# Kernel optimization log

Hardware: AMD Instinct MI355X
Metric: run time of the kernel (lower is better)

## Reference

```python
import jax, jax.numpy as jnp
import numpy as np

WS = 8      # window size
SS = 4      # shift size
NH = 4      # num heads
EPS = 1e-5
MLP_RATIO = 4


def _win_part(x, ws):
    # x: [B,D,H,W,C] -> [B*nD*nH*nW, ws^3, C]
    B, D, H, W, C = x.shape
    x = x.reshape(B, D // ws, ws, H // ws, ws, W // ws, ws, C)
    x = x.transpose(0, 1, 3, 5, 2, 4, 6, 7)
    return x.reshape(-1, ws * ws * ws, C)


def _win_rev(w, ws, B, D, H, W):
    C = w.shape[-1]
    x = w.reshape(B, D // ws, H // ws, W // ws, ws, ws, ws, C)
    x = x.transpose(0, 1, 4, 2, 5, 3, 6, 7)
    return x.reshape(B, D, H, W, C)


def _ln(x, g, b):
    m = jnp.mean(x, axis=-1, keepdims=True)
    v = jnp.mean((x - m) ** 2, axis=-1, keepdims=True)
    return (x - m) / jnp.sqrt(v + EPS) * g + b


def _rel_index(ws):
    coords = np.stack(np.meshgrid(np.arange(ws), np.arange(ws), np.arange(ws), indexing='ij'))  # [3,ws,ws,ws]
    cf = coords.reshape(3, -1)                      # [3, ws^3]
    rel = (cf[:, :, None] - cf[:, None, :]).transpose(1, 2, 0) + (ws - 1)  # [N,N,3]
    return rel[..., 0] * (2 * ws - 1) ** 2 + rel[..., 1] * (2 * ws - 1) + rel[..., 2]


def _attn_mask(D, H, W, ws, ss):
    img = np.zeros((1, D, H, W, 1), dtype=np.float32)
    cnt = 0
    sl = (slice(0, -ws), slice(-ws, -ss), slice(-ss, None))
    for d in sl:
        for h in sl:
            for w in sl:
                img[:, d, h, w, :] = cnt
                cnt += 1
    mw = np.asarray(_win_part(jnp.asarray(img), ws))[..., 0]  # [nW, ws^3]
    diff = mw[:, None, :] - mw[:, :, None]
    return np.where(diff != 0, -100.0, 0.0).astype(np.float32)


def setup_inputs() -> dict:
    key = jax.random.key(0)
    ks = jax.random.split(key, 12)
    B, D, H, W, C = 1, 16, 64, 64, 128
    mh = MLP_RATIO * C
    s = 0.02
    return {
        'x': jax.random.normal(ks[0], (B, D, H, W, C), jnp.float32),
        'attn_mask': jnp.asarray(_attn_mask(D, H, W, WS, SS)),
        'rel_index': jnp.asarray(_rel_index(WS), jnp.int32),
        'rel_bias': jax.random.normal(ks[1], ((2 * WS - 1) ** 3, NH), jnp.float32) * s,
        'qkv_w': jax.random.normal(ks[2], (3 * C, C), jnp.float32) * s,
        'qkv_b': jnp.zeros((3 * C,), jnp.float32),
        'proj_w': jax.random.normal(ks[3], (C, C), jnp.float32) * s,
        'proj_b': jnp.zeros((C,), jnp.float32),
        'norm1_g': jnp.ones((C,), jnp.float32),
        'norm1_b': jnp.zeros((C,), jnp.float32),
        'norm2_g': jnp.ones((C,), jnp.float32),
        'norm2_b': jnp.zeros((C,), jnp.float32),
        'mlp_w1': jax.random.normal(ks[4], (mh, C), jnp.float32) * s,
        'mlp_b1': jnp.zeros((mh,), jnp.float32),
        'mlp_w2': jax.random.normal(ks[5], (C, mh), jnp.float32) * s,
        'mlp_b2': jnp.zeros((C,), jnp.float32),
    }


def reference(x, attn_mask, rel_index, rel_bias, qkv_w, qkv_b, proj_w, proj_b,
              norm1_g, norm1_b, norm2_g, norm2_b, mlp_w1, mlp_b1, mlp_w2, mlp_b2):
    B, D, H, W, C = x.shape
    ws, ss, nh = WS, SS, NH
    hd = C // nh
    scale = hd ** -0.5
    N = ws ** 3
    shortcut = x
    h = _ln(x, norm1_g, norm1_b)
    h = jnp.roll(h, (-ss, -ss, -ss), axis=(1, 2, 3))
    xw = _win_part(h, ws)                 # [B_, N, C]
    B_ = xw.shape[0]
    nW = attn_mask.shape[0]
    qkv = xw @ qkv_w.T + qkv_b            # [B_, N, 3C]
    qkv = qkv.reshape(B_, N, 3, nh, hd).transpose(2, 0, 3, 1, 4)  # [3,B_,h,N,hd]
    q, k, v = qkv[0] * scale, qkv[1], qkv[2]
    attn = jnp.einsum('bhnd,bhmd->bhnm', q, k)
    rpe = rel_bias[rel_index.reshape(-1)].reshape(N, N, nh).transpose(2, 0, 1)  # [h,N,N]
    attn = attn + rpe[None]
    attn = attn.reshape(B_ // nW, nW, nh, N, N) + attn_mask[None, :, None]
    attn = jax.nn.softmax(attn.reshape(B_, nh, N, N), axis=-1)
    out = jnp.einsum('bhnm,bhmd->bhnd', attn, v).transpose(0, 2, 1, 3).reshape(B_, N, C)
    out = out @ proj_w.T + proj_b
    out = _win_rev(out, ws, B, D, H, W)
    out = jnp.roll(out, (ss, ss, ss), axis=(1, 2, 3))
    x = shortcut + out
    h2 = _ln(x, norm2_g, norm2_b)
    h2 = jax.nn.gelu(h2 @ mlp_w1.T + mlp_b1, approximate=False)
    return x + h2 @ mlp_w2.T + mlp_b2
```

## Files before the change

kernel.cpp:

```cpp
#include <hip/hip_runtime.h>
#include <math.h>

typedef __bf16 bf16;
typedef __bf16 bf16x4 __attribute__((ext_vector_type(4)));
typedef __bf16 bf16x8 __attribute__((ext_vector_type(8)));
typedef float f32x4 __attribute__((ext_vector_type(4)));
typedef unsigned short u16;
typedef u16 u16x2 __attribute__((ext_vector_type(2)));

#define LOG2E 1.4426950408889634f

__device__ __forceinline__ float b2f(u16 b) {
  return (float)__builtin_bit_cast(bf16, b);
}

__global__ void sniff_k(const unsigned* __restrict__ xw_, int* __restrict__ flag) {
  int lane = threadIdx.x;
  int c = 0;
#pragma unroll
  for (int j = 0; j < 4; j++) {
    unsigned e = (xw_[lane * 4 + j] >> 7) & 0xFFu;
    c += (e >= 100u && e <= 140u) ? 1 : 0;
  }
#pragma unroll
  for (int d = 1; d < 64; d <<= 1) c += __shfl_xor(c, d);
  if (lane == 0) *flag = (c >= 150) ? 1 : 0;
}

__global__ __launch_bounds__(256) void canon_big_k(const void* __restrict__ src,
                                                   bf16* __restrict__ dst,
                                                   const int* __restrict__ flag) {
  int i = (blockIdx.x * 256 + threadIdx.x) * 8;
  if (*flag) {
    *(bf16x8*)&dst[i] = *(const bf16x8*)((const bf16*)src + i);
  } else {
    const float* s = (const float*)src + i;
    bf16x8 v;
#pragma unroll
    for (int j = 0; j < 8; j++) v[j] = (bf16)s[j];
    *(bf16x8*)&dst[i] = v;
  }
}

struct CanonArgs {
  const void* src[13];
  bf16* dst[13];
  int n[13];
};

__global__ __launch_bounds__(256) void canon_small_k(CanonArgs a,
                                                     const int* __restrict__ flag) {
  int ti = blockIdx.y;
  int i = blockIdx.x * 256 + threadIdx.x;
  if (i >= a.n[ti]) return;
  if (*flag)
    a.dst[ti][i] = ((const bf16*)a.src[ti])[i];
  else
    a.dst[ti][i] = (bf16)((const float*)a.src[ti])[i];
}

__global__ __launch_bounds__(256) void rpem_k(const int* __restrict__ ridx,
                                              const bf16* __restrict__ rbias,
                                              bf16* __restrict__ rpem) {
  int t = blockIdx.x * 256 + threadIdx.x;
  int m0 = (t & 127) * 4, q = (t >> 7) & 511, h = (t >> 16) & 3, ty = t >> 18;
  int qd = q >> 6, qh = (q >> 3) & 7, qw = q & 7;
  int4 ri = *(const int4*)&ridx[q * 512 + m0];
  const int rv[4] = {ri.x, ri.y, ri.z, ri.w};
  bf16x4 o;
#pragma unroll
  for (int j = 0; j < 4; j++) {
    int m = m0 + j;
    int md = m >> 6, mh = (m >> 3) & 7, mw = m & 7;
    bool diff = ((ty & 4) && ((qd < 4) != (md < 4))) ||
                ((ty & 2) && ((qh < 4) != (mh < 4))) ||
                ((ty & 1) && ((qw < 4) != (mw < 4)));
    float v = (float)rbias[rv[j] * 4 + h] * LOG2E;
    o[j] = (bf16)(v + (diff ? -144.2695041f : 0.f));
  }
  *(bf16x4*)&rpem[(size_t)t * 4] = o;
}

template <int ROLL>
__global__ __launch_bounds__(256) void ln_k(const bf16* __restrict__ x,
                                            const bf16* __restrict__ g,
                                            const bf16* __restrict__ bsh,
                                            bf16* __restrict__ out) {
  int wave = threadIdx.x >> 6, lane = threadIdx.x & 63;
  int tok = blockIdx.x * 4 + wave;
  size_t src;
  if (ROLL) {
    int win = tok >> 9, pos = tok & 511;
    int rd = (win >> 6) * 8 + (pos >> 6);
    int rh = ((win >> 3) & 7) * 8 + ((pos >> 3) & 7);
    int rw = (win & 7) * 8 + (pos & 7);
    int od = (rd + 4) & 15, oh = (rh + 4) & 63, ow = (rw + 4) & 63;
    src = (size_t)((od * 64 + oh) * 64 + ow) * 128;
  } else {
    src = (size_t)tok * 128;
  }
  int ch = lane * 2;
  u16x2 xv = *(const u16x2*)(x + src + ch);
  float f0 = b2f(xv[0]), f1 = b2f(xv[1]);
  float s = f0 + f1, sq = f0 * f0 + f1 * f1;
#pragma unroll
  for (int d = 1; d < 64; d <<= 1) {
    s += __shfl_xor(s, d);
    sq += __shfl_xor(sq, d);
  }
  float mean = s * (1.f / 128.f);
  float var = sq * (1.f / 128.f) - mean * mean;
  float rstd = rsqrtf(fmaxf(var, 0.f) + 1e-5f);
  u16x2 gv = *(const u16x2*)(g + ch), bv = *(const u16x2*)(bsh + ch);
  u16x2 ov;
  ov[0] = __builtin_bit_cast(u16, (bf16)((f0 - mean) * rstd * b2f(gv[0]) + b2f(bv[0])));
  ov[1] = __builtin_bit_cast(u16, (bf16)((f1 - mean) * rstd * b2f(gv[1]) + b2f(bv[1])));
  *(u16x2*)(out + (size_t)tok * 128 + ch) = ov;
}

template <int EPI, int BM, int N_, int K_>
__global__ __launch_bounds__(256) void gemm_k(const bf16* __restrict__ A,
                                              const bf16* __restrict__ B,
                                              const bf16* __restrict__ bias,
                                              void* __restrict__ outv,
                                              const bf16* __restrict__ resid,
                                              const int* __restrict__ flag) {
  __shared__ __align__(16) u16 As[BM * 72];
  __shared__ __align__(16) u16 Bs[128 * 72];
  const int t = threadIdx.x;
  const int wave = t >> 6, lane = t & 63, l15 = lane & 15, quad = lane >> 4;
  const int m0 = blockIdx.x * BM, n0 = blockIdx.y * 128;
  constexpr int MI = BM / 32;
  constexpr int PA = BM / 32;
  int fl = 0;
  if constexpr (EPI == 3) fl = *flag;
  f32x4 acc[MI][4] = {};
  const int wr = (wave >> 1) * (BM / 2), wc = (wave & 1) * 64;
  const int srow = t >> 3, scol = (t & 7) * 8;
  constexpr int NC = K_ / 64;
  bf16x8 avA[PA], avB[PA];
#pragma unroll
  for (int p = 0; p < PA; p++) {
    int row = p * 32 + srow;
    avA[p] = *(const bf16x8*)(A + (size_t)(m0 + row) * K_ + scol);
  }
#pragma unroll
  for (int c = 0; c < NC; c++) {
    const bf16x8* av = (c & 1) ? avB : avA;
    bf16x8* avN = (c & 1) ? avA : avB;
    if (c + 1 < NC) {
#pragma unroll
      for (int p = 0; p < PA; p++) {
        int row = p * 32 + srow;
        avN[p] = *(const bf16x8*)(A + (size_t)(m0 + row) * K_ + (c + 1) * 64 + scol);
      }
    }
    bf16x8 bv[4];
#pragma unroll
    for (int p = 0; p < 4; p++) {
      int row = p * 32 + srow;
      bv[p] = *(const bf16x8*)(B + (size_t)(n0 + row) * K_ + c * 64 + scol);
    }
    __syncthreads();
#pragma unroll
    for (int p = 0; p < PA; p++)
      *(bf16x8*)&As[(p * 32 + srow) * 72 + scol] = av[p];
#pragma unroll
    for (int p = 0; p < 4; p++)
      *(bf16x8*)&Bs[(p * 32 + srow) * 72 + scol] = bv[p];
    __syncthreads();
#pragma unroll
    for (int ks = 0; ks < 2; ks++) {
      bf16x8 a[MI], b[4];
#pragma unroll
      for (int i = 0; i < MI; i++)
        a[i] = *(const bf16x8*)&As[(wr + i * 16 + l15) * 72 + ks * 32 + quad * 8];
#pragma unroll
      for (int j = 0; j < 4; j++)
        b[j] = *(const bf16x8*)&Bs[(wc + j * 16 + l15) * 72 + ks * 32 + quad * 8];
#pragma unroll
      for (int i = 0; i < MI; i++)
#pragma unroll
        for (int j = 0; j < 4; j++)
          acc[i][j] =
              __builtin_amdgcn_mfma_f32_16x16x32_bf16(a[i], b[j], acc[i][j], 0, 0, 0);
    }
  }
  const float qscale = 0.17677669529663687f * LOG2E;
#pragma unroll
  for (int i = 0; i < MI; i++) {
#pragma unroll
    for (int r = 0; r < 4; r++) {
      int tok = m0 + wr + i * 16 + quad * 4 + r;
      size_t obase = 0;
      if constexpr (EPI == 1) {
        int win = tok >> 9, pos = tok & 511;
        int rd = (win >> 6) * 8 + (pos >> 6);
        int rh = ((win >> 3) & 7) * 8 + ((pos >> 3) & 7);
        int rw = (win & 7) * 8 + (pos & 7);
        int od = (rd + 4) & 15, oh = (rh + 4) & 63, ow = (rw + 4) & 63;
        obase = (size_t)((od * 64 + oh) * 64 + ow) * 128;
      } else if constexpr (EPI != 0) {
        obase = (size_t)tok * N_;
      }
#pragma unroll
      for (int j = 0; j < 4; j++) {
        int gn = n0 + wc + j * 16 + l15;
        float v = acc[i][j][r] + (float)bias[gn];
        if constexpr (EPI == 0) {
          int tensor = gn >> 7, c = gn & 127, head = c >> 5, d = c & 31;
          if (tensor == 0) v *= qscale;
          int win = tok >> 9, pos = tok & 511;
          size_t off = ((((size_t)tensor * 4 + head) * 128 + win) * 512 + pos) * 32 + d;
          ((bf16*)outv)[off] = (bf16)v;
        } else if constexpr (EPI == 1) {
          v += (float)resid[obase + gn];
          ((bf16*)outv)[obase + gn] = (bf16)v;
        } else if constexpr (EPI == 2) {
          float v2 = v * v;
          float u2 = v * (2.30220806f + 0.10294323f * v2);
          float e2 = exp2f(u2);
          float rcp = __builtin_amdgcn_rcpf(e2 + 1.f);
          v = v - v * rcp;
          ((bf16*)outv)[obase + gn] = (bf16)v;
        } else {
          v += (float)resid[obase + gn];
          if (fl)
            ((bf16*)outv)[obase + gn] = (bf16)v;
          else
            ((float*)outv)[obase + gn] = v;
        }
      }
    }
  }
}

__global__ __launch_bounds__(512, 4) void attn_k(const bf16* __restrict__ qkv,
                                                 const bf16* __restrict__ rpem,
                                                 bf16* __restrict__ att) {
  __shared__ __align__(16) bf16 sVt[32 * 512];
  __shared__ __align__(16) bf16 sP[8][32 * 64];
  const int t = threadIdx.x;
  const int p = blockIdx.x;
  const int win = ((p >> 6) << 3) | (p & 7);
  const int mid = (p >> 3) & 7;
  const int head = mid >> 1, qh = mid & 1;
  const int wave = t >> 6, lane = t & 63, l15 = lane & 15, quad = lane >> 4;

  const int wd = win >> 6, wh = (win >> 3) & 7, ww = win & 7;
  const int type = ((wd == 1) << 2) | ((wh == 7) << 1) | (ww == 7);

  const size_t hw32 = (size_t)512 * 32;
  const bf16* qp = qkv + ((size_t)(0 * 4 + head) * 128 + win) * hw32;
  const bf16* kp = qkv + ((size_t)(1 * 4 + head) * 128 + win) * hw32;
  const bf16* vp = qkv + ((size_t)(2 * 4 + head) * 128 + win) * hw32;
  const bf16* rpeh = rpem + (size_t)(type * 4 + head) * 512 * 512;
  const int qbase = qh * 256 + wave * 32;

  {
    int kpi = t >> 3, dblk = (t & 7) * 4;
    char* sb = (char*)sVt;
#pragma unroll
    for (int kb = 0; kb < 4; kb++) {
      const bf16* v0 = vp + (size_t)(kb * 128 + 2 * kpi) * 32 + dblk;
      bf16x4 a = *(const bf16x4*)v0;
      bf16x4 b = *(const bf16x4*)(v0 + 32);
      int keyw = kb * 64 + kpi;
#pragma unroll
      for (int dd = 0; dd < 4; dd++) {
        int row = dblk + dd;
        unsigned wv = (unsigned)__builtin_bit_cast(u16, a[dd]) |
                      ((unsigned)__builtin_bit_cast(u16, b[dd]) << 16);
        *(unsigned*)(sb + ((row * 1024 + keyw * 4) ^ ((row & 7) << 4))) = wv;
      }
    }
  }

  bf16x8 qa[2];
#pragma unroll
  for (int nt = 0; nt < 2; nt++)
    qa[nt] = *(const bf16x8*)(qp + (size_t)(qbase + nt * 16 + l15) * 32 + quad * 8);

  bf16x8 ones;
#pragma unroll
  for (int e = 0; e < 8; e++) ones[e] = (bf16)1.0f;

  __syncthreads();

  f32x4 O[2][2] = {};
  f32x4 O2[2] = {};
  char* pw = (char*)sP[wave];
  const char* sv = (const char*)sVt;
  const int swz = (l15 & 7) << 4;

  auto load_tile = [&](int kt, bf16x8 (&kbv)[4], bf16x4 (&rvv)[4][2]) {
#pragma unroll
    for (int mt = 0; mt < 4; mt++) {
      kbv[mt] = *(const bf16x8*)(kp + (size_t)(kt * 64 + mt * 16 + l15) * 32 +
                                 quad * 8);
#pragma unroll
      for (int nt = 0; nt < 2; nt++)
        rvv[mt][nt] =
            *(const bf16x4*)(rpeh + (size_t)(qbase + nt * 16 + l15) * 512 +
                             kt * 64 + mt * 16 + quad * 4);
    }
  };

  auto compute_tile = [&](int kt, bf16x8 (&kbv)[4], bf16x4 (&rvv)[4][2]) {
    f32x4 S[4][2];
#pragma unroll
    for (int mt = 0; mt < 4; mt++)
#pragma unroll
      for (int nt = 0; nt < 2; nt++) {
        f32x4 c;
#pragma unroll
        for (int r = 0; r < 4; r++) c[r] = (float)rvv[mt][nt][r];
        S[mt][nt] =
            __builtin_amdgcn_mfma_f32_16x16x32_bf16(kbv[mt], qa[nt], c, 0, 0, 0);
      }
#pragma unroll
    for (int nt = 0; nt < 2; nt++)
#pragma unroll
      for (int mt = 0; mt < 4; mt++) {
        bf16x4 pv;
#pragma unroll
        for (int r = 0; r < 4; r++) pv[r] = (bf16)exp2f(S[mt][nt][r]);
        *(bf16x4*)(pw + (((nt * 16 + l15) * 128 + mt * 32 + quad * 8) ^ swz)) = pv;
      }
#pragma unroll
    for (int s = 0; s < 2; s++) {
      int vc = kt * 128 + s * 64 + quad * 16;
      int pc = s * 64 + quad * 16;
      bf16x8 va0 = *(const bf16x8*)(sv + ((l15 * 1024 + vc) ^ swz));
      bf16x8 va1 = *(const bf16x8*)(sv + (((16 + l15) * 1024 + vc) ^ swz));
      bf16x8 pb0 = *(const bf16x8*)(pw + ((l15 * 128 + pc) ^ swz));
      bf16x8 pb1 = *(const bf16x8*)(pw + (((16 + l15) * 128 + pc) ^ swz));
      O[0][0] = __builtin_amdgcn_mfma_f32_16x16x32_bf16(va0, pb0, O[0][0], 0, 0, 0);
      O[0][1] = __builtin_amdgcn_mfma_f32_16x16x32_bf16(va0, pb1, O[0][1], 0, 0, 0);
      O[1][0] = __builtin_amdgcn_mfma_f32_16x16x32_bf16(va1, pb0, O[1][0], 0, 0, 0);
      O[1][1] = __builtin_amdgcn_mfma_f32_16x16x32_bf16(va1, pb1, O[1][1], 0, 0, 0);
      O2[0] = __builtin_amdgcn_mfma_f32_16x16x32_bf16(ones, pb0, O2[0], 0, 0, 0);
      O2[1] = __builtin_amdgcn_mfma_f32_16x16x32_bf16(ones, pb1, O2[1], 0, 0, 0);
    }
  };

  bf16x8 kbA[4], kbB[4];
  bf16x4 rvA[4][2], rvB[4][2];
  load_tile(0, kbA, rvA);
#pragma unroll 1
  for (int i = 0; i < 4; i++) {
    int kt = 2 * i;
    load_tile(kt + 1, kbB, rvB);
    compute_tile(kt, kbA, rvA);
    if (kt + 2 < 8) load_tile(kt + 2, kbA, rvA);
    compute_tile(kt + 1, kbB, rvB);
  }
#pragma unroll
  for (int nt = 0; nt < 2; nt++) {
    float inv = __builtin_amdgcn_rcpf(O2[nt][0]);
    int q = qbase + nt * 16 + l15;
#pragma unroll
    for (int dm = 0; dm < 2; dm++) {
      bf16x4 o;
#pragma unroll
      for (int r = 0; r < 4; r++) o[r] = (bf16)(O[dm][nt][r] * inv);
      *(bf16x4*)(att + ((size_t)win * 512 + q) * 128 + head * 32 + dm * 16 +
                 quad * 4) = o;
    }
  }
}

extern "C" void kernel_launch(void* const* d_in, const int* in_sizes, int n_in,
                              void* d_out, int out_size, void* d_ws,
                              size_t ws_size, hipStream_t stream) {
  const int* rel_index = (const int*)d_in[2];
  char* w = (char*)d_ws;

  int* flag = (int*)w;
  bf16* rb_c = (bf16*)(w + (64ull << 10));
  bf16* qw_c = (bf16*)(w + (128ull << 10));
  bf16* pw_c = (bf16*)(w + (256ull << 10));
  bf16* w1_c = (bf16*)(w + (320ull << 10));
  bf16* w2_c = (bf16*)(w + (512ull << 10));
  bf16* qb_c = (bf16*)(w + (704ull << 10));
  bf16* pb_c = (bf16*)(w + (708ull << 10));
  bf16* g1_c = (bf16*)(w + (712ull << 10));
  bf16* b1n_c = (bf16*)(w + (716ull << 10));
  bf16* g2_c = (bf16*)(w + (720ull << 10));
  bf16* b2n_c = (bf16*)(w + (724ull << 10));
  bf16* mb1_c = (bf16*)(w + (728ull << 10));
  bf16* mb2_c = (bf16*)(w + (732ull << 10));
  bf16* x_c = (bf16*)(w + (1ull << 20));
  bf16* xw = (bf16*)(w + (17ull << 20));
  bf16* qkvb = (bf16*)(w + (33ull << 20));
  bf16* x2 = (bf16*)(w + (99ull << 20));
  bf16* rpem = x2;
  bf16* att = xw;
  bf16* h2 = xw;
  bf16* a1 = qkvb;

  sniff_k<<<1, 64, 0, stream>>>((const unsigned*)d_in[0], flag);
  canon_big_k<<<4096, 256, 0, stream>>>(d_in[0], x_c, flag);

  CanonArgs ca;
  const int srcidx[13] = {3, 4, 5, 6, 7, 8, 9, 10, 11, 12, 13, 14, 15};
  bf16* dsts[13] = {rb_c, qw_c, qb_c, pw_c, pb_c, g1_c, b1n_c,
                    g2_c, b2n_c, w1_c, mb1_c, w2_c, mb2_c};
  for (int i = 0; i < 13; i++) {
    ca.src[i] = d_in[srcidx[i]];
    ca.dst[i] = dsts[i];
    ca.n[i] = in_sizes[srcidx[i]];
  }
  canon_small_k<<<dim3(256, 13), 256, 0, stream>>>(ca, flag);

  rpem_k<<<8192, 256, 0, stream>>>(rel_index, rb_c, rpem);
  ln_k<1><<<16384, 256, 0, stream>>>(x_c, g1_c, b1n_c, xw);
  gemm_k<0, 128, 384, 128><<<dim3(512, 3), 256, 0, stream>>>(xw, qw_c, qb_c,
                                                             qkvb, nullptr, flag);
  attn_k<<<1024, 512, 0, stream>>>(qkvb, rpem, att);
  gemm_k<1, 64, 128, 128><<<dim3(1024, 1), 256, 0, stream>>>(att, pw_c, pb_c,
                                                             x2, x_c, flag);
  ln_k<0><<<16384, 256, 0, stream>>>(x2, g2_c, b2n_c, h2);
  gemm_k<2, 128, 512, 128><<<dim3(512, 4), 256, 0, stream>>>(h2, w1_c, mb1_c,
                                                             a1, nullptr, flag);
  gemm_k<3, 64, 128, 512><<<dim3(1024, 1), 256, 0, stream>>>(a1, w2_c, mb2_c,
                                                             d_out, x2, flag);
}
```

Baseline: 422.1 us.

## Stage GEMM tiles via direct global-to-LDS loads with double buffering; simplify attention loop

The GEMM kernel now copies A and B tiles straight from global memory into a double-buffered, XOR-swizzled shared-memory array with global_load_lds. This replaces the register-staged copy and the padded layout, so the next K-chunk loads while the current one is multiplied, with one barrier per chunk. The cost is a larger shared-memory footprint, which may lower occupancy. Separately, the attention kernel drops its manual two-tile register prefetch of K and relative-bias values for a plain per-tile loop, which lowers register pressure but gives up explicit load overlap.

```diff
diff --git a/kernel.cpp b/kernel.cpp
--- a/kernel.cpp
+++ b/kernel.cpp
@@ -125,59 +125,58 @@
                                               void* __restrict__ outv,
                                               const bf16* __restrict__ resid,
                                               const int* __restrict__ flag) {
-  __shared__ __align__(16) u16 As[BM * 72];
-  __shared__ __align__(16) u16 Bs[128 * 72];
+  __shared__ __align__(16) u16 SM[2][(BM + 128) * 64];
   const int t = threadIdx.x;
   const int wave = t >> 6, lane = t & 63, l15 = lane & 15, quad = lane >> 4;
   const int m0 = blockIdx.x * BM, n0 = blockIdx.y * 128;
   constexpr int MI = BM / 32;
-  constexpr int PA = BM / 32;
+  constexpr int NC = K_ / 64;
+  constexpr int PASSES = (BM + 128) / 32;
   int fl = 0;
   if constexpr (EPI == 3) fl = *flag;
   f32x4 acc[MI][4] = {};
   const int wr = (wave >> 1) * (BM / 2), wc = (wave & 1) * 64;
-  const int srow = t >> 3, scol = (t & 7) * 8;
-  constexpr int NC = K_ / 64;
-  bf16x8 avA[PA], avB[PA];
-#pragma unroll
-  for (int p = 0; p < PA; p++) {
-    int row = p * 32 + srow;
-    avA[p] = *(const bf16x8*)(A + (size_t)(m0 + row) * K_ + scol);
-  }
+  const int srow = t >> 3;
+  const int sc16 = t & 7;
+
+  auto stage = [&](int c, int buf) {
+#pragma unroll
+    for (int p = 0; p < PASSES; p++) {
+      int row = p * 32 + srow;
+      int cs = sc16 ^ (row & 7);
+      const u16* src;
+      if (row < BM)
+        src = (const u16*)A + (size_t)(m0 + row) * K_ + c * 64 + cs * 8;
+      else
+        src = (const u16*)B + (size_t)(n0 + row - BM) * K_ + c * 64 + cs * 8;
+      __builtin_amdgcn_global_load_lds(
+          (const __attribute__((address_space(1))) void*)src,
+          (__attribute__((address_space(3))) void*)&SM[buf][row * 64 + sc16 * 8],
+          16, 0, 0);
+    }
+  };
+
+  stage(0, 0);
+  __syncthreads();
 #pragma unroll
   for (int c = 0; c < NC; c++) {
-    const bf16x8* av = (c & 1) ? avB : avA;
-    bf16x8* avN = (c & 1) ? avA : avB;
-    if (c + 1 < NC) {
-#pragma unroll
-      for (int p = 0; p < PA; p++) {
-        int row = p * 32 + srow;
-        avN[p] = *(const bf16x8*)(A + (size_t)(m0 + row) * K_ + (c + 1) * 64 + scol);
-      }
-    }
-    bf16x8 bv[4];
-#pragma unroll
-    for (int p = 0; p < 4; p++) {
-      int row = p * 32 + srow;
-      bv[p] = *(const bf16x8*)(B + (size_t)(n0 + row) * K_ + c * 64 + scol);
-    }
-    __syncthreads();
-#pragma unroll
-    for (int p = 0; p < PA; p++)
-      *(bf16x8*)&As[(p * 32 + srow) * 72 + scol] = av[p];
-#pragma unroll
-    for (int p = 0; p < 4; p++)
-      *(bf16x8*)&Bs[(p * 32 + srow) * 72 + scol] = bv[p];
-    __syncthreads();
+    if (c + 1 < NC) stage(c + 1, (c + 1) & 1);
+    const char* cur = (const char*)SM[c & 1];
 #pragma unroll
     for (int ks = 0; ks < 2; ks++) {
       bf16x8 a[MI], b[4];
 #pragma unroll
-      for (int i = 0; i < MI; i++)
-        a[i] = *(const bf16x8*)&As[(wr + i * 16 + l15) * 72 + ks * 32 + quad * 8];
-#pragma unroll
-      for (int j = 0; j < 4; j++)
-        b[j] = *(const bf16x8*)&Bs[(wc + j * 16 + l15) * 72 + ks * 32 + quad * 8];
+      for (int i = 0; i < MI; i++) {
+        int row = wr + i * 16 + l15;
+        a[i] = *(const bf16x8*)(cur + row * 128 +
+                                (((ks * 4 + quad) ^ (row & 7)) << 4));
+      }
+#pragma unroll
+      for (int j = 0; j < 4; j++) {
+        int row = BM + wc + j * 16 + l15;
+        b[j] = *(const bf16x8*)(cur + row * 128 +
+                                (((ks * 4 + quad) ^ (row & 7)) << 4));
+      }
 #pragma unroll
       for (int i = 0; i < MI; i++)
 #pragma unroll
@@ -185,6 +184,7 @@
           acc[i][j] =
               __builtin_amdgcn_mfma_f32_16x16x32_bf16(a[i], b[j], acc[i][j], 0, 0, 0);
     }
+    if (c + 1 < NC) __syncthreads();
   }
   const float qscale = 0.17677669529663687f * LOG2E;
 #pragma unroll
@@ -293,20 +293,20 @@
   const char* sv = (const char*)sVt;
   const int swz = (l15 & 7) << 4;
 
-  auto load_tile = [&](int kt, bf16x8 (&kbv)[4], bf16x4 (&rvv)[4][2]) {
+#pragma unroll 1
+  for (int kt = 0; kt < 8; kt++) {
+    bf16x8 kb[4];
+    bf16x4 rv[4][2];
 #pragma unroll
     for (int mt = 0; mt < 4; mt++) {
-      kbv[mt] = *(const bf16x8*)(kp + (size_t)(kt * 64 + mt * 16 + l15) * 32 +
-                                 quad * 8);
+      kb[mt] = *(const bf16x8*)(kp + (size_t)(kt * 64 + mt * 16 + l15) * 32 +
+                                quad * 8);
 #pragma unroll
       for (int nt = 0; nt < 2; nt++)
-        rvv[mt][nt] =
+        rv[mt][nt] =
             *(const bf16x4*)(rpeh + (size_t)(qbase + nt * 16 + l15) * 512 +
                              kt * 64 + mt * 16 + quad * 4);
     }
-  };
-
-  auto compute_tile = [&](int kt, bf16x8 (&kbv)[4], bf16x4 (&rvv)[4][2]) {
     f32x4 S[4][2];
 #pragma unroll
     for (int mt = 0; mt < 4; mt++)
@@ -314,9 +314,8 @@
       for (int nt = 0; nt < 2; nt++) {
         f32x4 c;
 #pragma unroll
-        for (int r = 0; r < 4; r++) c[r] = (float)rvv[mt][nt][r];
-        S[mt][nt] =
-            __builtin_amdgcn_mfma_f32_16x16x32_bf16(kbv[mt], qa[nt], c, 0, 0, 0);
+        for (int r = 0; r < 4; r++) c[r] = (float)rv[mt][nt][r];
+        S[mt][nt] = __builtin_amdgcn_mfma_f32_16x16x32_bf16(kb[mt], qa[nt], c, 0, 0, 0);
       }
 #pragma unroll
     for (int nt = 0; nt < 2; nt++)
@@ -342,18 +341,6 @@
       O2[0] = __builtin_amdgcn_mfma_f32_16x16x32_bf16(ones, pb0, O2[0], 0, 0, 0);
       O2[1] = __builtin_amdgcn_mfma_f32_16x16x32_bf16(ones, pb1, O2[1], 0, 0, 0);
     }
-  };
-
-  bf16x8 kbA[4], kbB[4];
-  bf16x4 rvA[4][2], rvB[4][2];
-  load_tile(0, kbA, rvA);
-#pragma unroll 1
-  for (int i = 0; i < 4; i++) {
-    int kt = 2 * i;
-    load_tile(kt + 1, kbB, rvB);
-    compute_tile(kt, kbA, rvA);
-    if (kt + 2 < 8) load_tile(kt + 2, kbA, rvA);
-    compute_tile(kt + 1, kbB, rvB);
   }
 #pragma unroll
   for (int nt = 0; nt < 2; nt++) {
```

Result: no change. 414.6 us (-1.8%).
